# Kernel tuning notes

Hardware: AMD Instinct MI355X
Metric: run time of the kernel (lower is better)

## Reference

```python
import jax, jax.numpy as jnp
from jax import lax
import numpy as np

# Dims: batch, input channels (=3*C), output channels, kernel size, spatial
B, CIN, C, K, H, W = 8, 576, 192, 3, 56, 56
KK = K * K  # number of kernel positions


def setup_inputs() -> dict:
    key = jax.random.key(0)
    k1, k2, k3, k4 = jax.random.split(key, 4)
    x = jax.random.normal(k1, (B, CIN, H, W), jnp.float32)
    # 1x1 conv producing per-channel, per-position dynamic logits (C*KK outputs)
    fc_w = jax.random.normal(k2, (C * KK, CIN), jnp.float32) * 0.05
    # per-position grouped conv kernels: (KK, C_out, CIN//C=3, K, K)
    w1 = jax.random.normal(k3, (KK, C, CIN // C, K, K), jnp.float32) * 0.1
    # per-position depthwise conv kernels: (KK, C, K, K)
    w2 = jax.random.normal(k4, (KK, C, K, K), jnp.float32) * 0.1
    return {"x": x, "fc_w": fc_w, "w1": w1, "w2": w2}


def reference(x, fc_w, w1, w2):
    b = x.shape[0]
    # dynamic softmax weights over the KK kernel positions: (b, C, KK, H, W)
    logits = jnp.einsum('oc,bchw->bohw', fc_w, x).reshape(b, C, KK, H, W)
    attn = jax.nn.softmax(logits, axis=2)

    # dep_conv1: per-position grouped conv (3C -> C, groups=C), vmapped over KK
    def conv1(wi):  # wi: (C, 3, K, K)
        return lax.conv_general_dilated(x, wi, (1, 1), 'SAME',
                                        feature_group_count=C)

    feat = jax.nn.relu(jax.vmap(conv1)(w1))  # (KK, b, C, H, W)

    # dep_conv2: per-position depthwise conv (C -> C, groups=C)
    def conv2(fi, wi):  # fi: (b, C, H, W), wi: (C, K, K)
        return lax.conv_general_dilated(fi, wi[:, None], (1, 1), 'SAME',
                                        feature_group_count=C)

    out_pos = jax.vmap(conv2)(feat, w2)  # (KK, b, C, H, W)

    # softmax-weighted aggregation over kernel positions
    out = jnp.einsum('ibchw,bcihw->bchw', out_pos, attn)  # (b, C, H, W)
    return out
```

## Files before the change

### kernel.cpp

```cpp
#include <hip/hip_runtime.h>
#include <hip/hip_bf16.h>

constexpr int Bn   = 8;
constexpr int Cin  = 576;
constexpr int Cc   = 192;
constexpr int Hh   = 56;
constexpr int Ww   = 56;
constexpr int HWn  = Hh * Ww;
constexpr int CKK  = Cc * 9;

constexpr int GM = 1792;
constexpr int GK = 576;
constexpr int GN = Bn * HWn;

using f16x8 = __attribute__((ext_vector_type(8))) _Float16;
using f32x4 = __attribute__((ext_vector_type(4))) float;

__device__ __forceinline__ void async_copy16(void* lds, const void* gptr) {
    __builtin_amdgcn_global_load_lds(
        (const __attribute__((address_space(1))) unsigned int*)gptr,
        (__attribute__((address_space(3))) unsigned int*)lds, 16, 0, 0);
}

__device__ __forceinline__ float blo(unsigned int u) { return __uint_as_float(u << 16); }
__device__ __forceinline__ float bhi(unsigned int u) { return __uint_as_float(u & 0xffff0000u); }
__device__ __forceinline__ unsigned short bf16bits(float f) {
    union { __hip_bfloat16 h; unsigned short u; } c; c.h = __float2bfloat16(f); return c.u;
}

__global__ __launch_bounds__(256) void cast_fcw_kernel(
    const float* __restrict__ fcw, _Float16* __restrict__ out)
{
    int idx = blockIdx.x * 256 + threadIdx.x;
    int e = idx * 4;
    if (e >= GM * GK) return;
    int row = e / GK;
    union { ushort4 u; _Float16 h[4]; } pk;
    if (row < CKK) {
        float4 v = *(const float4*)&fcw[e];
        pk.h[0] = (_Float16)v.x; pk.h[1] = (_Float16)v.y;
        pk.h[2] = (_Float16)v.z; pk.h[3] = (_Float16)v.w;
    } else {
        pk.h[0] = pk.h[1] = pk.h[2] = pk.h[3] = (_Float16)0.f;
    }
    *(ushort4*)&out[e] = pk.u;
}

__global__ __launch_bounds__(256) void transpose_cast_kernel(
    const float* __restrict__ x, _Float16* __restrict__ xt)
{
    __shared__ float t[32][65];
    const int b = blockIdx.z, k0 = blockIdx.y * 32, hw0 = blockIdx.x * 64;
    const int tid = threadIdx.x;
    const int col = tid & 63, kr = tid >> 6;
#pragma unroll
    for (int p = 0; p < 8; p++) {
        int k = kr + p * 4;
        t[k][col] = x[(size_t)(b * Cin + k0 + k) * HWn + hw0 + col];
    }
    __syncthreads();
    const int row = tid >> 2, cq = (tid & 3) * 8;
    union { uint4 u; _Float16 h[8]; } pk;
#pragma unroll
    for (int j = 0; j < 8; j++) pk.h[j] = (_Float16)t[cq + j][row];
    *(uint4*)&xt[(size_t)(b * HWn + hw0 + row) * GK + k0 + cq] = pk.u;
}

__global__ __launch_bounds__(256) void gemm_mfma_kernel(
    const _Float16* __restrict__ A, const _Float16* __restrict__ Bm,
    __hip_bfloat16* __restrict__ logits)
{
    __shared__ _Float16 As[128 * 32];
    __shared__ _Float16 Bs[128 * 32];

    const int tid = threadIdx.x;
    const int n0 = blockIdx.x * 128;
    const int m0 = blockIdx.y * 128;
    const int lane = tid & 63;
    const int wave = tid >> 6;
    const int wm = (wave >> 1) * 64;
    const int wn = (wave & 1) * 64;
    const int lm = lane & 15;
    const int lc = lane >> 4;

    const int lrow = tid >> 2;
    const int koff = (((tid & 3) ^ ((tid >> 3) & 3)) << 3);

    int offA[4], offB[4];
#pragma unroll
    for (int i = 0; i < 4; i++) {
        int ra = wm + i * 16 + lm;
        offA[i] = ra * 32 + ((lc ^ ((ra >> 1) & 3)) << 3);
        int rb = wn + i * 16 + lm;
        offB[i] = rb * 32 + ((lc ^ ((rb >> 1) & 3)) << 3);
    }

    f32x4 acc[4][4] = {};

    for (int k0 = 0; k0 < GK; k0 += 32) {
        async_copy16(&As[(size_t)tid * 8],        &A[(size_t)(m0 + lrow) * GK + k0 + koff]);
        async_copy16(&As[2048 + (size_t)tid * 8], &A[(size_t)(m0 + 64 + lrow) * GK + k0 + koff]);
        async_copy16(&Bs[(size_t)tid * 8],        &Bm[(size_t)(n0 + lrow) * GK + k0 + koff]);
        async_copy16(&Bs[2048 + (size_t)tid * 8], &Bm[(size_t)(n0 + 64 + lrow) * GK + k0 + koff]);
        __syncthreads();
        f16x8 af[4], bf[4];
#pragma unroll
        for (int i = 0; i < 4; i++) {
            af[i] = *(const f16x8*)&As[offA[i]];
            bf[i] = *(const f16x8*)&Bs[offB[i]];
        }
#pragma unroll
        for (int i = 0; i < 4; i++)
#pragma unroll
            for (int j = 0; j < 4; j++)
                acc[i][j] = __builtin_amdgcn_mfma_f32_16x16x32_f16(bf[j], af[i], acc[i][j], 0, 0, 0);
        __syncthreads();
    }

    const int mcol = m0 + wm + lm;
#pragma unroll
    for (int i = 0; i < 4; i++) {
        int m = mcol + i * 16;
        if (m >= CKK) continue;
#pragma unroll
        for (int j = 0; j < 4; j++) {
            int n = n0 + wn + j * 16 + lc * 4;
            int b = n / HWn, hw = n - b * HWn;
            uint2 pk;
            pk.x = (unsigned)bf16bits(acc[i][j][0]) | ((unsigned)bf16bits(acc[i][j][1]) << 16);
            pk.y = (unsigned)bf16bits(acc[i][j][2]) | ((unsigned)bf16bits(acc[i][j][3]) << 16);
            *(uint2*)&logits[((size_t)b * CKK + m) * HWn + hw] = pk;
        }
    }
}

__global__ __launch_bounds__(256, 3) void conv1_kernel(
    const float* __restrict__ x, const float* __restrict__ w1,
    __hip_bfloat16* __restrict__ feat)
{
    const int c = blockIdx.x, hb = blockIdx.y, b = blockIdx.z;
    const int tid = threadIdx.x;
    const int h0 = hb * 28;
    __shared__ float xt[3][30][60];

    for (int idx = tid; idx < 1260; idx += 256) {
        int d = idx / 420, rem = idx - d * 420;
        int r = rem / 14, g = rem - r * 14;
        int h = h0 - 1 + r;
        float4 v = {0.f, 0.f, 0.f, 0.f};
        if (h >= 0 && h < Hh)
            v = *(const float4*)&x[((size_t)(b * Cin + 3 * c + d) * Hh + h) * Ww + 4 * g];
        xt[d][r][1 + 4 * g + 0] = v.x;
        xt[d][r][1 + 4 * g + 1] = v.y;
        xt[d][r][1 + 4 * g + 2] = v.z;
        xt[d][r][1 + 4 * g + 3] = v.w;
    }
    for (int idx = tid; idx < 180; idx += 256) {
        int d = idx / 60, rem = idx - d * 60;
        int r = rem >> 1, col = (rem & 1) ? 57 : 0;
        xt[d][r][col] = 0.f;
    }
    __syncthreads();

    if (tid < 196) {
        const int row = tid / 7, seg = tid - (tid / 7) * 7;
        const int w0 = seg * 8;

        float win[3][3][10];
#pragma unroll
        for (int d = 0; d < 3; d++)
#pragma unroll
            for (int u = 0; u < 3; u++)
#pragma unroll
                for (int k = 0; k < 10; k++)
                    win[d][u][k] = xt[d][row + u][w0 + k];

        const int hw = (h0 + row) * Ww + w0;
#pragma unroll 1
        for (int i = 0; i < 9; i++) {
            const float* wp = w1 + ((size_t)i * Cc + c) * 27;
            float wgt[27];
#pragma unroll
            for (int j = 0; j < 27; j++) wgt[j] = wp[j];
            float acc[8] = {};
#pragma unroll
            for (int d = 0; d < 3; d++)
#pragma unroll
                for (int u = 0; u < 3; u++)
#pragma unroll
                    for (int v = 0; v < 3; v++) {
                        float wv = wgt[d * 9 + u * 3 + v];
#pragma unroll
                        for (int p = 0; p < 8; p++)
                            acc[p] += win[d][u][p + v] * wv;
                    }
            uint4 pk;
            pk.x = (unsigned)bf16bits(fmaxf(acc[0], 0.f)) | ((unsigned)bf16bits(fmaxf(acc[1], 0.f)) << 16);
            pk.y = (unsigned)bf16bits(fmaxf(acc[2], 0.f)) | ((unsigned)bf16bits(fmaxf(acc[3], 0.f)) << 16);
            pk.z = (unsigned)bf16bits(fmaxf(acc[4], 0.f)) | ((unsigned)bf16bits(fmaxf(acc[5], 0.f)) << 16);
            pk.w = (unsigned)bf16bits(fmaxf(acc[6], 0.f)) | ((unsigned)bf16bits(fmaxf(acc[7], 0.f)) << 16);
            *(uint4*)&feat[(((size_t)i * Bn + b) * Cc + c) * HWn + hw] = pk;
        }
    }
}

__global__ __launch_bounds__(256, 3) void conv2_agg_kernel(
    const __hip_bfloat16* __restrict__ feat,
    const __hip_bfloat16* __restrict__ logits,
    const float* __restrict__ w2, float* __restrict__ out)
{
    const int c = blockIdx.x, hb = blockIdx.y, b = blockIdx.z;
    const int tid = threadIdx.x;
    const int h0 = hb * 28;
    __shared__ unsigned short ft[9][30][72];

    for (int idx = tid; idx < 1890; idx += 256) {
        int i = idx / 210, rem = idx - i * 210;
        int r = rem / 7, g = rem - r * 7;
        int h = h0 - 1 + r;
        uint4 v = {0u, 0u, 0u, 0u};
        if (h >= 0 && h < Hh)
            v = *(const uint4*)&feat[(((size_t)i * Bn + b) * Cc + c) * HWn + h * Ww + 8 * g];
        unsigned int* dst = (unsigned int*)&ft[i][r][2 + 8 * g];
        dst[0] = v.x; dst[1] = v.y; dst[2] = v.z; dst[3] = v.w;
    }
    for (int idx = tid; idx < 1080; idx += 256) {
        int i = idx / 120, rem = idx - i * 120;
        int r = rem >> 2, e = rem & 3;
        int col = (e < 2) ? e : 56 + e;
        ft[i][r][col] = 0;
    }
    __syncthreads();

    if (tid < 196) {
        const int row = tid / 7, seg = tid - (tid / 7) * 7;
        const int w0 = 8 * seg;
        const int hw = (h0 + row) * Ww + w0;

        float lg[9][8];
        const __hip_bfloat16* lbase = logits + ((size_t)b * CKK + c * 9) * HWn + hw;
#pragma unroll
        for (int i = 0; i < 9; i++) {
            uint4 lv = *(const uint4*)&lbase[(size_t)i * HWn];
            lg[i][0] = blo(lv.x); lg[i][1] = bhi(lv.x);
            lg[i][2] = blo(lv.y); lg[i][3] = bhi(lv.y);
            lg[i][4] = blo(lv.z); lg[i][5] = bhi(lv.z);
            lg[i][6] = blo(lv.w); lg[i][7] = bhi(lv.w);
        }
#pragma unroll
        for (int p = 0; p < 8; p++) {
            float mx = lg[0][p];
#pragma unroll
            for (int i = 1; i < 9; i++) mx = fmaxf(mx, lg[i][p]);
            float sum = 0.f;
#pragma unroll
            for (int i = 0; i < 9; i++) { lg[i][p] = __expf(lg[i][p] - mx); sum += lg[i][p]; }
            float inv = __builtin_amdgcn_rcpf(sum);
#pragma unroll
            for (int i = 0; i < 9; i++) lg[i][p] *= inv;
        }

        float oacc[8] = {};
#pragma unroll
        for (int i = 0; i < 9; i++) {
            const float* wp = w2 + ((size_t)i * Cc + c) * 9;
            float wgt[9];
#pragma unroll
            for (int j = 0; j < 9; j++) wgt[j] = wp[j];
            float cacc[8] = {};
#pragma unroll
            for (int u = 0; u < 3; u++) {
                const unsigned short* fr = &ft[i][row + u][w0];
                uint4 a = *(const uint4*)fr;
                uint2 bq = *(const uint2*)(fr + 8);
                float wf[11];
                wf[1] = bhi(a.x);
                wf[2] = blo(a.y);  wf[3] = bhi(a.y);
                wf[4] = blo(a.z);  wf[5] = bhi(a.z);
                wf[6] = blo(a.w);  wf[7] = bhi(a.w);
                wf[8] = blo(bq.x); wf[9] = bhi(bq.x);
                wf[10] = blo(bq.y);
#pragma unroll
                for (int v = 0; v < 3; v++) {
                    float wv = wgt[u * 3 + v];
#pragma unroll
                    for (int p = 0; p < 8; p++)
                        cacc[p] += wf[p + v + 1] * wv;
                }
            }
#pragma unroll
            for (int p = 0; p < 8; p++) oacc[p] += cacc[p] * lg[i][p];
        }

        float* obase = out + ((size_t)(b * Cc + c)) * HWn + hw;
        float4 o0, o1;
        o0.x = oacc[0]; o0.y = oacc[1]; o0.z = oacc[2]; o0.w = oacc[3];
        o1.x = oacc[4]; o1.y = oacc[5]; o1.z = oacc[6]; o1.w = oacc[7];
        *(float4*)&obase[0] = o0;
        *(float4*)&obase[4] = o1;
    }
}

extern "C" void kernel_launch(void* const* d_in, const int* in_sizes, int n_in,
                              void* d_out, int out_size, void* d_ws, size_t ws_size,
                              hipStream_t stream)
{
    const float* x    = (const float*)d_in[0];
    const float* fc_w = (const float*)d_in[1];
    const float* w1   = (const float*)d_in[2];
    const float* w2   = (const float*)d_in[3];
    float* out = (float*)d_out;

    char* ws = (char*)d_ws;
    __hip_bfloat16* logits = (__hip_bfloat16*)ws;
    char* region2 = ws + (size_t)Bn * CKK * HWn * 2;
    __hip_bfloat16* feat = (__hip_bfloat16*)region2;
    _Float16* xt    = (_Float16*)region2;
    _Float16* fcw16 = (_Float16*)(region2 + (size_t)GN * GK * 2);

    cast_fcw_kernel<<<(GM * GK / 4 + 255) / 256, 256, 0, stream>>>(fc_w, fcw16);
    transpose_cast_kernel<<<dim3(HWn / 64, GK / 32, Bn), 256, 0, stream>>>(x, xt);
    gemm_mfma_kernel<<<dim3(GN / 128, GM / 128), 256, 0, stream>>>(fcw16, xt, logits);
    conv1_kernel<<<dim3(Cc, 2, Bn), 256, 0, stream>>>(x, w1, feat);
    conv2_agg_kernel<<<dim3(Cc, 2, Bn), 256, 0, stream>>>(feat, logits, w2, out);
}
```

Before: 306.0 us.

## Fuse grouped conv1 and depthwise conv2 aggregation into one kernel via LDS

```diff
diff --git a/kernel.cpp b/kernel.cpp
--- a/kernel.cpp
+++ b/kernel.cpp
@@ -74,8 +74,8 @@
     __shared__ _Float16 Bs[128 * 32];
 
     const int tid = threadIdx.x;
-    const int n0 = blockIdx.x * 128;
-    const int m0 = blockIdx.y * 128;
+    const int m0 = blockIdx.x * 128;
+    const int n0 = blockIdx.y * 128;
     const int lane = tid & 63;
     const int wave = tid >> 6;
     const int wm = (wave >> 1) * 64;
@@ -134,19 +134,22 @@
     }
 }
 
-__global__ __launch_bounds__(256, 3) void conv1_kernel(
+__global__ __launch_bounds__(256) void conv_fused_kernel(
     const float* __restrict__ x, const float* __restrict__ w1,
-    __hip_bfloat16* __restrict__ feat)
+    const __hip_bfloat16* __restrict__ logits,
+    const float* __restrict__ w2, float* __restrict__ out)
 {
     const int c = blockIdx.x, hb = blockIdx.y, b = blockIdx.z;
     const int tid = threadIdx.x;
     const int h0 = hb * 28;
-    __shared__ float xt[3][30][60];
-
-    for (int idx = tid; idx < 1260; idx += 256) {
-        int d = idx / 420, rem = idx - d * 420;
+
+    __shared__ float xt[3][32][60];
+    __shared__ unsigned short ft[9][30][72];
+
+    for (int idx = tid; idx < 1344; idx += 256) {
+        int d = idx / 448, rem = idx - d * 448;
         int r = rem / 14, g = rem - r * 14;
-        int h = h0 - 1 + r;
+        int h = h0 - 2 + r;
         float4 v = {0.f, 0.f, 0.f, 0.f};
         if (h >= 0 && h < Hh)
             v = *(const float4*)&x[((size_t)(b * Cin + 3 * c + d) * Hh + h) * Ww + 4 * g];
@@ -155,16 +158,18 @@
         xt[d][r][1 + 4 * g + 2] = v.z;
         xt[d][r][1 + 4 * g + 3] = v.w;
     }
-    for (int idx = tid; idx < 180; idx += 256) {
-        int d = idx / 60, rem = idx - d * 60;
+    for (int idx = tid; idx < 192; idx += 256) {
+        int d = idx / 64, rem = idx - d * 64;
         int r = rem >> 1, col = (rem & 1) ? 57 : 0;
         xt[d][r][col] = 0.f;
     }
     __syncthreads();
 
-    if (tid < 196) {
+    if (tid < 210) {
         const int row = tid / 7, seg = tid - (tid / 7) * 7;
         const int w0 = seg * 8;
+        const int fh = h0 - 1 + row;
+        const bool valid = (fh >= 0) && (fh < Hh);
 
         float win[3][3][10];
 #pragma unroll
@@ -175,7 +180,6 @@
                 for (int k = 0; k < 10; k++)
                     win[d][u][k] = xt[d][row + u][w0 + k];
 
-        const int hw = (h0 + row) * Ww + w0;
 #pragma unroll 1
         for (int i = 0; i < 9; i++) {
             const float* wp = w1 + ((size_t)i * Cc + c) * 27;
@@ -194,35 +198,18 @@
                         for (int p = 0; p < 8; p++)
                             acc[p] += win[d][u][p + v] * wv;
                     }
-            uint4 pk;
-            pk.x = (unsigned)bf16bits(fmaxf(acc[0], 0.f)) | ((unsigned)bf16bits(fmaxf(acc[1], 0.f)) << 16);
-            pk.y = (unsigned)bf16bits(fmaxf(acc[2], 0.f)) | ((unsigned)bf16bits(fmaxf(acc[3], 0.f)) << 16);
-            pk.z = (unsigned)bf16bits(fmaxf(acc[4], 0.f)) | ((unsigned)bf16bits(fmaxf(acc[5], 0.f)) << 16);
-            pk.w = (unsigned)bf16bits(fmaxf(acc[6], 0.f)) | ((unsigned)bf16bits(fmaxf(acc[7], 0.f)) << 16);
-            *(uint4*)&feat[(((size_t)i * Bn + b) * Cc + c) * HWn + hw] = pk;
-        }
-    }
-}
-
-__global__ __launch_bounds__(256, 3) void conv2_agg_kernel(
-    const __hip_bfloat16* __restrict__ feat,
-    const __hip_bfloat16* __restrict__ logits,
-    const float* __restrict__ w2, float* __restrict__ out)
-{
-    const int c = blockIdx.x, hb = blockIdx.y, b = blockIdx.z;
-    const int tid = threadIdx.x;
-    const int h0 = hb * 28;
-    __shared__ unsigned short ft[9][30][72];
-
-    for (int idx = tid; idx < 1890; idx += 256) {
-        int i = idx / 210, rem = idx - i * 210;
-        int r = rem / 7, g = rem - r * 7;
-        int h = h0 - 1 + r;
-        uint4 v = {0u, 0u, 0u, 0u};
-        if (h >= 0 && h < Hh)
-            v = *(const uint4*)&feat[(((size_t)i * Bn + b) * Cc + c) * HWn + h * Ww + 8 * g];
-        unsigned int* dst = (unsigned int*)&ft[i][r][2 + 8 * g];
-        dst[0] = v.x; dst[1] = v.y; dst[2] = v.z; dst[3] = v.w;
+            unsigned int pk[4];
+            if (valid) {
+#pragma unroll
+                for (int q = 0; q < 4; q++)
+                    pk[q] = (unsigned)bf16bits(fmaxf(acc[2 * q], 0.f)) |
+                            ((unsigned)bf16bits(fmaxf(acc[2 * q + 1], 0.f)) << 16);
+            } else {
+                pk[0] = pk[1] = pk[2] = pk[3] = 0u;
+            }
+            unsigned int* dst = (unsigned int*)&ft[i][row][2 + w0];
+            dst[0] = pk[0]; dst[1] = pk[1]; dst[2] = pk[2]; dst[3] = pk[3];
+        }
     }
     for (int idx = tid; idx < 1080; idx += 256) {
         int i = idx / 120, rem = idx - i * 120;
@@ -313,14 +300,11 @@
 
     char* ws = (char*)d_ws;
     __hip_bfloat16* logits = (__hip_bfloat16*)ws;
-    char* region2 = ws + (size_t)Bn * CKK * HWn * 2;
-    __hip_bfloat16* feat = (__hip_bfloat16*)region2;
-    _Float16* xt    = (_Float16*)region2;
-    _Float16* fcw16 = (_Float16*)(region2 + (size_t)GN * GK * 2);
+    _Float16* xt    = (_Float16*)(ws + (size_t)Bn * CKK * HWn * 2);
+    _Float16* fcw16 = (_Float16*)(ws + (size_t)Bn * CKK * HWn * 2 + (size_t)GN * GK * 2);
 
     cast_fcw_kernel<<<(GM * GK / 4 + 255) / 256, 256, 0, stream>>>(fc_w, fcw16);
     transpose_cast_kernel<<<dim3(HWn / 64, GK / 32, Bn), 256, 0, stream>>>(x, xt);
-    gemm_mfma_kernel<<<dim3(GN / 128, GM / 128), 256, 0, stream>>>(fcw16, xt, logits);
-    conv1_kernel<<<dim3(Cc, 2, Bn), 256, 0, stream>>>(x, w1, feat);
-    conv2_agg_kernel<<<dim3(Cc, 2, Bn), 256, 0, stream>>>(feat, logits, w2, out);
-}
+    gemm_mfma_kernel<<<dim3(GM / 128, GN / 128), 256, 0, stream>>>(fcw16, xt, logits);
+    conv_fused_kernel<<<dim3(Cc, 2, Bn), 256, 0, stream>>>(x, w1, logits, w2, out);
+}
```

Measured after the change: 359.6 us. 17.5% more time.
